# Performance work log

Hardware: AMD Instinct MI355X
Metric: run time of the kernel (lower is better)

Reference implementation:

```python
import jax, jax.numpy as jnp
import numpy as np
from jax import lax

IMG_SIZE = 512        # efficientdet-d0 input resolution
TOP_K = 256           # fixed candidate count for jit-compatible NMS
THRESHOLD = 0.01      # score threshold (init kwarg)
IOU_THRESHOLD = 0.5   # NMS IoU threshold (init kwarg)


def make_anchors():
    """Standard EfficientDet-d0 anchors: P3-P7, 3 scales x 3 ratios, xyxy."""
    strides = [8, 16, 32, 64, 128]
    scales = [2.0 ** 0, 2.0 ** (1.0 / 3.0), 2.0 ** (2.0 / 3.0)]
    ratios = [0.5, 1.0, 2.0]
    base = 4.0
    out = []
    for s in strides:
        fs = IMG_SIZE // s
        xs = (np.arange(fs, dtype=np.float32) + 0.5) * s
        cy, cx = np.meshgrid(xs, xs, indexing='ij')
        for r in ratios:
            for sc in scales:
                w = base * s * sc * np.sqrt(1.0 / r)
                h = base * s * sc * np.sqrt(r)
                a = np.stack([cx - w / 2, cy - h / 2, cx + w / 2, cy + h / 2], -1)
                out.append(a.reshape(-1, 4))
    return np.concatenate(out, 0).astype(np.float32)  # [49104, 4]


def decode_boxes(anchors, regs):
    """RetinaNet-style delta decode. anchors [A,4] xyxy, regs [B,A,4]."""
    aw = anchors[:, 2] - anchors[:, 0]
    ah = anchors[:, 3] - anchors[:, 1]
    acx = anchors[:, 0] + 0.5 * aw
    acy = anchors[:, 1] + 0.5 * ah
    dx, dy, dw, dh = regs[..., 0], regs[..., 1], regs[..., 2], regs[..., 3]
    cx = acx + dx * aw
    cy = acy + dy * ah
    w = aw * jnp.exp(jnp.clip(dw, -4.0, 4.0))
    h = ah * jnp.exp(jnp.clip(dh, -4.0, 4.0))
    boxes = jnp.stack([cx - 0.5 * w, cy - 0.5 * h, cx + 0.5 * w, cy + 0.5 * h], -1)
    return jnp.clip(boxes, 0.0, float(IMG_SIZE))  # [B,A,4]


def pairwise_iou(boxes):
    """boxes [K,4] xyxy -> iou [K,K]."""
    area = jnp.maximum(boxes[:, 2] - boxes[:, 0], 0) * jnp.maximum(boxes[:, 3] - boxes[:, 1], 0)
    lt = jnp.maximum(boxes[:, None, :2], boxes[None, :, :2])
    rb = jnp.minimum(boxes[:, None, 2:], boxes[None, :, 2:])
    wh = jnp.maximum(rb - lt, 0.0)
    inter = wh[..., 0] * wh[..., 1]
    union = area[:, None] + area[None, :] - inter
    return inter / jnp.maximum(union, 1e-8)


def nms_keep(boxes, scores):
    """Sequential NMS over score-sorted candidates. boxes [K,4], scores [K]."""
    K = boxes.shape[0]
    iou = pairwise_iou(boxes)  # [K,K]
    ar = jnp.arange(K)
    keep0 = scores > 0.0

    def body(i, keep):
        suppressed = jnp.any(keep & (iou[:, i] > IOU_THRESHOLD) & (ar < i))
        return keep.at[i].set(keep[i] & ~suppressed)

    return lax.fori_loop(0, K, body, keep0)


def setup_inputs() -> dict:
    key = jax.random.key(0)
    k1, k2 = jax.random.split(key)
    B, A, C = 8, 49104, 80
    cls_logits = jax.random.normal(k1, (B, A, C), dtype=jnp.float32) - 2.0
    box_regs = 0.2 * jax.random.normal(k2, (B, A, 4), dtype=jnp.float32)
    anchors = jnp.asarray(make_anchors())
    return {"cls_logits": cls_logits, "box_regs": box_regs, "anchors": anchors}


def reference(cls_logits, box_regs, anchors):
    probs = jax.nn.sigmoid(cls_logits)            # [B,A,C]
    scores = probs.max(-1)                        # [B,A]
    labels = probs.argmax(-1)                     # [B,A]
    boxes = decode_boxes(anchors, box_regs)       # [B,A,4]
    scores = jnp.where(scores > THRESHOLD, scores, 0.0)
    top_s, idx = lax.top_k(scores, TOP_K)         # [B,K]
    top_b = jnp.take_along_axis(boxes, idx[..., None], axis=1)   # [B,K,4]
    top_l = jnp.take_along_axis(labels, idx, axis=1)             # [B,K]
    keep = jax.vmap(nms_keep)(top_b, top_s)                      # [B,K] bool
    keep_f = keep.astype(top_b.dtype)
    dets = jnp.concatenate([top_b * keep_f[..., None], (top_s * keep_f)[..., None]], -1)  # [B,K,5]
    return dets, top_l, keep
```

## Files before the change

### kernel.cpp

```cpp
#include <hip/hip_runtime.h>
#include <stdint.h>
#include <math.h>

#define IMGF   512.0f
#define A_N    49104
#define B_N    8
#define C_N    80
#define K_N    256
#define IOU_T  0.5f
#define NBIN   4096
#define CAP    2048

__device__ __forceinline__ int bin_of(uint32_t key) {
    float s = __uint_as_float(key);
    int b = (int)(s * 4096.0f);
    return b > 4095 ? 4095 : b;
}

__global__ __launch_bounds__(256) void score_kernel(
    const float* __restrict__ logits,
    uint32_t* __restrict__ keys)
{
    const int tid  = threadIdx.x;
    const int lane = tid & 63;
    const int grp  = lane >> 2, j = lane & 3;
    const int g = blockIdx.x * 64 + (tid >> 6) * 16 + grp;

    const float4* p = (const float4*)(logits + (size_t)g * C_N);
    float4 v0 = p[j], v1 = p[j + 4], v2 = p[j + 8], v3 = p[j + 12], v4 = p[j + 16];
    float m = fmaxf(fmaxf(fmaxf(v0.x, v0.y), fmaxf(v0.z, v0.w)),
                    fmaxf(fmaxf(v1.x, v1.y), fmaxf(v1.z, v1.w)));
    m = fmaxf(m, fmaxf(fmaxf(v2.x, v2.y), fmaxf(v2.z, v2.w)));
    m = fmaxf(m, fmaxf(fmaxf(v3.x, v3.y), fmaxf(v3.z, v3.w)));
    m = fmaxf(m, fmaxf(fmaxf(v4.x, v4.y), fmaxf(v4.z, v4.w)));
    m = fmaxf(m, __shfl_xor(m, 1, 64));
    m = fmaxf(m, __shfl_xor(m, 2, 64));
    if (j == 0) {
        float s = 1.0f / (1.0f + expf(-m));
        if (!(s > 0.01f)) s = 0.0f;
        keys[g] = __float_as_uint(s);
    }
}

__global__ __launch_bounds__(1024) void select_nms_kernel(
    const uint32_t* __restrict__ keys,
    const float* __restrict__ logits,
    const float* __restrict__ regs,
    const float* __restrict__ anchors,
    float* __restrict__ out)
{
    const int b   = blockIdx.x;
    const int tid = threadIdx.x;
    const int lane = tid & 63, wv = tid >> 6;

    __shared__ uint32_t hist[NBIN];
    __shared__ int wtots[16];
    __shared__ int sh_T, sh_nc;
    __shared__ unsigned long long cand[CAP];
    __shared__ unsigned long long sorted[K_N];
    __shared__ float4 sbox[K_N];
    __shared__ float  sscore[K_N];
    __shared__ int    slab[K_N];
    __shared__ unsigned long long supr[K_N][4];
    __shared__ unsigned long long keepw[4];

    const uint32_t* kb = keys + (size_t)b * A_N;
    const uint4* kb4 = (const uint4*)kb;
    const int N4 = A_N / 4;

    for (int i = tid; i < NBIN; i += 1024) hist[i] = 0;
    if (tid == 0) sh_nc = 0;
    __syncthreads();
    for (int i = tid; i < N4; i += 1024) {
        uint4 v = kb4[i];
        atomicAdd(&hist[bin_of(v.x)], 1u);
        atomicAdd(&hist[bin_of(v.y)], 1u);
        atomicAdd(&hist[bin_of(v.z)], 1u);
        atomicAdd(&hist[bin_of(v.w)], 1u);
    }
    __syncthreads();

    const int lo = tid * 4;
    int seg = (int)hist[lo] + (int)hist[lo + 1]
            + (int)hist[lo + 2] + (int)hist[lo + 3];
    int s1 = seg;
#pragma unroll
    for (int off = 1; off < 64; off <<= 1) {
        int v = __shfl_down(s1, off, 64);
        if (lane + off < 64) s1 += v;
    }
    if (lane == 0) wtots[wv] = s1;
    __syncthreads();
    int wsuf = 0;
    for (int w = wv + 1; w < 16; ++w) wsuf += wtots[w];
    int above = wsuf + (s1 - seg);
    if (above < K_N && above + seg >= K_N) {
        int cum = above;
        for (int bin = lo + 3; bin >= lo; --bin) {
            int c = (int)hist[bin];
            if (cum + c >= K_N) { sh_T = bin; break; }
            cum += c;
        }
    }
    __syncthreads();
    const int T = sh_T;

    for (int i = tid; i < N4; i += 1024) {
        uint4 v = kb4[i];
        uint32_t ks[4] = { v.x, v.y, v.z, v.w };
#pragma unroll
        for (int q = 0; q < 4; ++q) {
            if (bin_of(ks[q]) >= T) {
                int p = atomicAdd(&sh_nc, 1);
                if (p < CAP)
                    cand[p] = ((unsigned long long)ks[q] << 32)
                            | (unsigned long long)(0xFFFFFFFFu - (uint32_t)(4 * i + q));
            }
        }
    }
    if (tid < K_N) sorted[tid] = 0ull;
    __syncthreads();
    int nc = sh_nc; if (nc > CAP) nc = CAP;

    for (int i = tid; i < nc; i += 1024) {
        unsigned long long me = cand[i];
        int r = 0;
        for (int jq = 0; jq < nc; ++jq) r += (cand[jq] > me);
        if (r < K_N) sorted[r] = me;
    }
    __syncthreads();

    if (tid < K_N) {
#pragma clang fp contract(off)
        unsigned long long cv = sorted[tid];
        uint32_t key = (uint32_t)(cv >> 32);
        uint32_t ai  = 0xFFFFFFFFu - (uint32_t)cv;
        if (ai >= (uint32_t)A_N) ai = 0;
        int a = (int)ai;
        float s = __uint_as_float(key);
        sscore[tid] = s;

        {
            const float4* lp = (const float4*)(logits + ((size_t)b * A_N + a) * C_N);
            float best = -INFINITY; int cls = 0;
#pragma unroll
            for (int k = 0; k < 20; ++k) {
                float4 w = lp[k];
                if (w.x > best) { best = w.x; cls = 4 * k + 0; }
                if (w.y > best) { best = w.y; cls = 4 * k + 1; }
                if (w.z > best) { best = w.z; cls = 4 * k + 2; }
                if (w.w > best) { best = w.w; cls = 4 * k + 3; }
            }
            slab[tid] = cls;
        }

        float ax0 = anchors[4 * a + 0], ay0 = anchors[4 * a + 1];
        float ax1 = anchors[4 * a + 2], ay1 = anchors[4 * a + 3];
        float aw = ax1 - ax0, ah = ay1 - ay0;
        float acx = ax0 + 0.5f * aw, acy = ay0 + 0.5f * ah;
        const float* r = regs + ((size_t)b * A_N + a) * 4;
        float dx = r[0], dy = r[1], dw = r[2], dh = r[3];
        float cx = acx + dx * aw;
        float cy = acy + dy * ah;
        dw = fminf(fmaxf(dw, -4.0f), 4.0f);
        dh = fminf(fmaxf(dh, -4.0f), 4.0f);
        float w = aw * expf(dw);
        float h = ah * expf(dh);
        float x0 = cx - 0.5f * w, y0 = cy - 0.5f * h;
        float x1 = cx + 0.5f * w, y1 = cy + 0.5f * h;
        x0 = fminf(fmaxf(x0, 0.0f), IMGF);
        y0 = fminf(fmaxf(y0, 0.0f), IMGF);
        x1 = fminf(fmaxf(x1, 0.0f), IMGF);
        y1 = fminf(fmaxf(y1, 0.0f), IMGF);
        sbox[tid] = make_float4(x0, y0, x1, y1);
    }
    __syncthreads();

    {
#pragma clang fp contract(off)
        const int row = tid & 255, gq = tid >> 8;
        float4 bi = sbox[row];
        float areai = fmaxf(bi.z - bi.x, 0.0f) * fmaxf(bi.w - bi.y, 0.0f);
        unsigned long long m = 0;
        const int jlo = gq * 64, jhi = jlo + 64;
        int start = row + 1 > jlo ? row + 1 : jlo;
        for (int jx = start; jx < jhi; ++jx) {
            float4 bj = sbox[jx];
            float areaj = fmaxf(bj.z - bj.x, 0.0f) * fmaxf(bj.w - bj.y, 0.0f);
            float lx = fmaxf(bi.x, bj.x), ly = fmaxf(bi.y, bj.y);
            float rx = fminf(bi.z, bj.z), ry = fminf(bi.w, bj.w);
            float iw = fmaxf(rx - lx, 0.0f), ih = fmaxf(ry - ly, 0.0f);
            float inter = iw * ih;
            float uni = areai + areaj - inter;
            float iou = inter / fmaxf(uni, 1e-8f);
            if (iou > IOU_T) m |= 1ull << (jx & 63);
        }
        supr[row][gq] = m;
    }
    if (tid < K_N) {
        unsigned long long ball = __ballot(sscore[tid] > 0.0f);
        if ((tid & 63) == 0) keepw[tid >> 6] = ball;
    }
    __syncthreads();

    if (tid == 0) {
        unsigned long long k0 = keepw[0], k1 = keepw[1], k2 = keepw[2], k3 = keepw[3];
#define NMS_CHUNK(c, kc)                                                     \
        for (int l = 0; l < 64; ++l) {                                       \
            const int i = (c) * 64 + l;                                      \
            unsigned long long w0 = supr[i][0], w1 = supr[i][1];             \
            unsigned long long w2 = supr[i][2], w3 = supr[i][3];             \
            if ((kc >> l) & 1ull) {                                          \
                k0 &= ~w0; k1 &= ~w1; k2 &= ~w2; k3 &= ~w3;                  \
            }                                                                \
        }
        NMS_CHUNK(0, k0)
        NMS_CHUNK(1, k1)
        NMS_CHUNK(2, k2)
        NMS_CHUNK(3, k3)
#undef NMS_CHUNK
        keepw[0] = k0; keepw[1] = k1; keepw[2] = k2; keepw[3] = k3;
    }
    __syncthreads();

    if (tid < K_N) {
        float keepf = ((keepw[tid >> 6] >> (tid & 63)) & 1ull) ? 1.0f : 0.0f;
        float4 bx = sbox[tid];
        float s = sscore[tid];
        float* det = out + ((size_t)b * K_N + tid) * 5;
        det[0] = bx.x * keepf;
        det[1] = bx.y * keepf;
        det[2] = bx.z * keepf;
        det[3] = bx.w * keepf;
        det[4] = s * keepf;
        out[(size_t)B_N * K_N * 5 + (size_t)b * K_N + tid] = (float)slab[tid];
        out[(size_t)B_N * K_N * 5 + (size_t)B_N * K_N + (size_t)b * K_N + tid] = keepf;
    }
}

extern "C" void kernel_launch(void* const* d_in, const int* in_sizes, int n_in,
                              void* d_out, int out_size, void* d_ws, size_t ws_size,
                              hipStream_t stream)
{
    const float* logits  = (const float*)d_in[0];
    const float* regs    = (const float*)d_in[1];
    const float* anchors = (const float*)d_in[2];
    float* out = (float*)d_out;

    uint32_t* keys = (uint32_t*)d_ws;

    const int total = B_N * A_N;
    score_kernel<<<total / 64, 256, 0, stream>>>(logits, keys);
    select_nms_kernel<<<B_N, 1024, 0, stream>>>(keys, logits, regs, anchors, out);
}
```

Before: 237.8 us.

## Fuse score and select/NMS kernels into one cooperative kernel with grid sync

Merges the scoring kernel and the per-batch select/NMS kernel into a single cooperative launch of 512 blocks of 256 threads, separated by a grid-wide sync. This removes one kernel launch and the gap between kernels. In exchange, the selection and NMS phase now runs with 256 threads per batch instead of 1024, so the histogram, candidate scan, rank sort and IoU loops each do more serial work per thread. It also requires all 512 blocks to be co-resident.

```diff
diff --git a/kernel.cpp b/kernel.cpp
--- a/kernel.cpp
+++ b/kernel.cpp
@@ -1,6 +1,9 @@
 #include <hip/hip_runtime.h>
+#include <hip/hip_cooperative_groups.h>
 #include <stdint.h>
 #include <math.h>
+
+namespace cg = cooperative_groups;
 
 #define IMGF   512.0f
 #define A_N    49104
@@ -10,6 +13,8 @@
 #define IOU_T  0.5f
 #define NBIN   4096
 #define CAP    2048
+#define NBLK   512
+#define NCHUNK (B_N * A_N / 64)
 
 __device__ __forceinline__ int bin_of(uint32_t key) {
     float s = __uint_as_float(key);
@@ -17,44 +22,19 @@
     return b > 4095 ? 4095 : b;
 }
 
-__global__ __launch_bounds__(256) void score_kernel(
-    const float* __restrict__ logits,
-    uint32_t* __restrict__ keys)
-{
-    const int tid  = threadIdx.x;
-    const int lane = tid & 63;
-    const int grp  = lane >> 2, j = lane & 3;
-    const int g = blockIdx.x * 64 + (tid >> 6) * 16 + grp;
-
-    const float4* p = (const float4*)(logits + (size_t)g * C_N);
-    float4 v0 = p[j], v1 = p[j + 4], v2 = p[j + 8], v3 = p[j + 12], v4 = p[j + 16];
-    float m = fmaxf(fmaxf(fmaxf(v0.x, v0.y), fmaxf(v0.z, v0.w)),
-                    fmaxf(fmaxf(v1.x, v1.y), fmaxf(v1.z, v1.w)));
-    m = fmaxf(m, fmaxf(fmaxf(v2.x, v2.y), fmaxf(v2.z, v2.w)));
-    m = fmaxf(m, fmaxf(fmaxf(v3.x, v3.y), fmaxf(v3.z, v3.w)));
-    m = fmaxf(m, fmaxf(fmaxf(v4.x, v4.y), fmaxf(v4.z, v4.w)));
-    m = fmaxf(m, __shfl_xor(m, 1, 64));
-    m = fmaxf(m, __shfl_xor(m, 2, 64));
-    if (j == 0) {
-        float s = 1.0f / (1.0f + expf(-m));
-        if (!(s > 0.01f)) s = 0.0f;
-        keys[g] = __float_as_uint(s);
-    }
-}
-
-__global__ __launch_bounds__(1024) void select_nms_kernel(
-    const uint32_t* __restrict__ keys,
+__global__ __launch_bounds__(256) void fused_kernel(
     const float* __restrict__ logits,
     const float* __restrict__ regs,
     const float* __restrict__ anchors,
+    uint32_t* __restrict__ keys,
     float* __restrict__ out)
 {
-    const int b   = blockIdx.x;
-    const int tid = threadIdx.x;
+    const int tid  = threadIdx.x;
     const int lane = tid & 63, wv = tid >> 6;
+    const int grp  = lane >> 2, j = lane & 3;
 
     __shared__ uint32_t hist[NBIN];
-    __shared__ int wtots[16];
+    __shared__ int wtots[4];
     __shared__ int sh_T, sh_nc;
     __shared__ unsigned long long cand[CAP];
     __shared__ unsigned long long sorted[K_N];
@@ -64,14 +44,39 @@
     __shared__ unsigned long long supr[K_N][4];
     __shared__ unsigned long long keepw[4];
 
+    for (int c = blockIdx.x; c < NCHUNK; c += NBLK) {
+        const int g = c * 64 + wv * 16 + grp;
+        const float4* p = (const float4*)(logits + (size_t)g * C_N);
+        float4 v0 = p[j], v1 = p[j + 4], v2 = p[j + 8],
+               v3 = p[j + 12], v4 = p[j + 16];
+        float m = fmaxf(fmaxf(fmaxf(v0.x, v0.y), fmaxf(v0.z, v0.w)),
+                        fmaxf(fmaxf(v1.x, v1.y), fmaxf(v1.z, v1.w)));
+        m = fmaxf(m, fmaxf(fmaxf(v2.x, v2.y), fmaxf(v2.z, v2.w)));
+        m = fmaxf(m, fmaxf(fmaxf(v3.x, v3.y), fmaxf(v3.z, v3.w)));
+        m = fmaxf(m, fmaxf(fmaxf(v4.x, v4.y), fmaxf(v4.z, v4.w)));
+        m = fmaxf(m, __shfl_xor(m, 1, 64));
+        m = fmaxf(m, __shfl_xor(m, 2, 64));
+        if (j == 0) {
+            float s = 1.0f / (1.0f + expf(-m));
+            if (!(s > 0.01f)) s = 0.0f;
+            keys[g] = __float_as_uint(s);
+        }
+    }
+
+    __threadfence();
+    cg::this_grid().sync();
+    if (blockIdx.x >= B_N) return;
+    __threadfence();
+
+    const int b = blockIdx.x;
     const uint32_t* kb = keys + (size_t)b * A_N;
     const uint4* kb4 = (const uint4*)kb;
     const int N4 = A_N / 4;
 
-    for (int i = tid; i < NBIN; i += 1024) hist[i] = 0;
+    for (int i = tid; i < NBIN; i += 256) hist[i] = 0;
     if (tid == 0) sh_nc = 0;
     __syncthreads();
-    for (int i = tid; i < N4; i += 1024) {
+    for (int i = tid; i < N4; i += 256) {
         uint4 v = kb4[i];
         atomicAdd(&hist[bin_of(v.x)], 1u);
         atomicAdd(&hist[bin_of(v.y)], 1u);
@@ -80,9 +85,10 @@
     }
     __syncthreads();
 
-    const int lo = tid * 4;
-    int seg = (int)hist[lo] + (int)hist[lo + 1]
-            + (int)hist[lo + 2] + (int)hist[lo + 3];
+    const int lo = tid * 16;
+    int seg = 0;
+#pragma unroll
+    for (int q = 0; q < 16; ++q) seg += (int)hist[lo + q];
     int s1 = seg;
 #pragma unroll
     for (int off = 1; off < 64; off <<= 1) {
@@ -92,11 +98,11 @@
     if (lane == 0) wtots[wv] = s1;
     __syncthreads();
     int wsuf = 0;
-    for (int w = wv + 1; w < 16; ++w) wsuf += wtots[w];
+    for (int w = wv + 1; w < 4; ++w) wsuf += wtots[w];
     int above = wsuf + (s1 - seg);
     if (above < K_N && above + seg >= K_N) {
         int cum = above;
-        for (int bin = lo + 3; bin >= lo; --bin) {
+        for (int bin = lo + 15; bin >= lo; --bin) {
             int c = (int)hist[bin];
             if (cum + c >= K_N) { sh_T = bin; break; }
             cum += c;
@@ -105,7 +111,7 @@
     __syncthreads();
     const int T = sh_T;
 
-    for (int i = tid; i < N4; i += 1024) {
+    for (int i = tid; i < N4; i += 256) {
         uint4 v = kb4[i];
         uint32_t ks[4] = { v.x, v.y, v.z, v.w };
 #pragma unroll
@@ -122,7 +128,7 @@
     __syncthreads();
     int nc = sh_nc; if (nc > CAP) nc = CAP;
 
-    for (int i = tid; i < nc; i += 1024) {
+    for (int i = tid; i < nc; i += 256) {
         unsigned long long me = cand[i];
         int r = 0;
         for (int jq = 0; jq < nc; ++jq) r += (cand[jq] > me);
@@ -130,7 +136,7 @@
     }
     __syncthreads();
 
-    if (tid < K_N) {
+    {
 #pragma clang fp contract(off)
         unsigned long long cv = sorted[tid];
         uint32_t key = (uint32_t)(cv >> 32);
@@ -178,13 +184,10 @@
 
     {
 #pragma clang fp contract(off)
-        const int row = tid & 255, gq = tid >> 8;
-        float4 bi = sbox[row];
+        float4 bi = sbox[tid];
         float areai = fmaxf(bi.z - bi.x, 0.0f) * fmaxf(bi.w - bi.y, 0.0f);
-        unsigned long long m = 0;
-        const int jlo = gq * 64, jhi = jlo + 64;
-        int start = row + 1 > jlo ? row + 1 : jlo;
-        for (int jx = start; jx < jhi; ++jx) {
+        unsigned long long m0 = 0, m1 = 0, m2 = 0, m3 = 0;
+        for (int jx = tid + 1; jx < K_N; ++jx) {
             float4 bj = sbox[jx];
             float areaj = fmaxf(bj.z - bj.x, 0.0f) * fmaxf(bj.w - bj.y, 0.0f);
             float lx = fmaxf(bi.x, bj.x), ly = fmaxf(bi.y, bj.y);
@@ -193,11 +196,19 @@
             float inter = iw * ih;
             float uni = areai + areaj - inter;
             float iou = inter / fmaxf(uni, 1e-8f);
-            if (iou > IOU_T) m |= 1ull << (jx & 63);
-        }
-        supr[row][gq] = m;
-    }
-    if (tid < K_N) {
+            if (iou > IOU_T) {
+                unsigned long long bit = 1ull << (jx & 63);
+                switch (jx >> 6) {
+                    case 0: m0 |= bit; break;
+                    case 1: m1 |= bit; break;
+                    case 2: m2 |= bit; break;
+                    default: m3 |= bit; break;
+                }
+            }
+        }
+        supr[tid][0] = m0; supr[tid][1] = m1; supr[tid][2] = m2; supr[tid][3] = m3;
+    }
+    {
         unsigned long long ball = __ballot(sscore[tid] > 0.0f);
         if ((tid & 63) == 0) keepw[tid >> 6] = ball;
     }
@@ -223,7 +234,7 @@
     }
     __syncthreads();
 
-    if (tid < K_N) {
+    {
         float keepf = ((keepw[tid >> 6] >> (tid & 63)) & 1ull) ? 1.0f : 0.0f;
         float4 bx = sbox[tid];
         float s = sscore[tid];
@@ -246,10 +257,10 @@
     const float* regs    = (const float*)d_in[1];
     const float* anchors = (const float*)d_in[2];
     float* out = (float*)d_out;
-
     uint32_t* keys = (uint32_t*)d_ws;
 
-    const int total = B_N * A_N;
-    score_kernel<<<total / 64, 256, 0, stream>>>(logits, keys);
-    select_nms_kernel<<<B_N, 1024, 0, stream>>>(keys, logits, regs, anchors, out);
+    void* args[] = { (void*)&logits, (void*)&regs, (void*)&anchors,
+                     (void*)&keys, (void*)&out };
+    hipLaunchCooperativeKernel((const void*)fused_kernel,
+                               dim3(NBLK), dim3(256), args, 0, stream);
 }
```

After: 372.5 us. 1.57x slower.
